# Kernel tuning notes

Hardware: AMD Instinct MI355X
Metric: run time of the kernel (lower is better)

Reference implementation:

```python
import math
import jax, jax.numpy as jnp
import numpy as np

D_MODEL = 1024
N_HEADS = 16
D_K = D_MODEL // N_HEADS
THETA = 10000.0


def setup_inputs() -> dict:
    key = jax.random.key(0)
    k1, k2, k3 = jax.random.split(key, 3)
    B, S = 2, 2048
    x = jax.random.normal(k1, (B, S, D_MODEL), dtype=jnp.float32)
    std_qkv = math.sqrt(2.0 / (D_MODEL + 3 * D_MODEL))
    std_out = math.sqrt(2.0 / (D_MODEL + D_MODEL))
    # Linear weights stored as (out_features, in_features) to match the
    # einsum '... i, o i -> ... o' contraction (trunc-normal approximated
    # by clipped normal for the reference baseline).
    w_qkv = jnp.clip(jax.random.normal(k2, (3 * D_MODEL, D_MODEL), dtype=jnp.float32) * std_qkv,
                     -3 * std_qkv, 3 * std_qkv)
    b_qkv = jnp.zeros((3 * D_MODEL,), dtype=jnp.float32)
    w_out = jnp.clip(jax.random.normal(k3, (D_MODEL, D_MODEL), dtype=jnp.float32) * std_out,
                     -3 * std_out, 3 * std_out)
    b_out = jnp.zeros((D_MODEL,), dtype=jnp.float32)
    return {"x": x, "w_qkv": w_qkv, "b_qkv": b_qkv, "w_out": w_out, "b_out": b_out}


def _rope(t, cos, sin):
    # t: (B, H, S, D_K); cos/sin: (S, D_K//2) broadcast over batch/heads.
    B, H, S, d = t.shape
    tp = t.reshape(B, H, S, d // 2, 2)
    even, odd = tp[..., 0], tp[..., 1]
    r_even = even * cos - odd * sin
    r_odd = even * sin + odd * cos
    return jnp.stack([r_even, r_odd], axis=-1).reshape(B, H, S, d)


def reference(x, w_qkv, b_qkv, w_out, b_out):
    B, S, _ = x.shape
    # QKV projection: weight is (out, in)
    qkv = jnp.einsum('bsi,oi->bso', x, w_qkv) + b_qkv  # (B, S, 3*D_MODEL)
    qkv = qkv.reshape(B, S, 3, N_HEADS, D_K).transpose(2, 0, 3, 1, 4)  # (3, B, H, S, D_K)
    q, k, v = qkv[0], qkv[1], qkv[2]

    # RoPE with default token_positions = arange(S)
    inv_freq = THETA ** (-(jnp.arange(0, D_K, 2, dtype=jnp.float32)) / D_K)  # (D_K//2,)
    ang = jnp.arange(S, dtype=jnp.float32)[:, None] * inv_freq[None, :]      # (S, D_K//2)
    cos, sin = jnp.cos(ang), jnp.sin(ang)
    q = _rope(q, cos, sin)
    k = _rope(k, cos, sin)

    # Scaled dot-product attention in fp32 with causal mask
    scale = 1.0 / math.sqrt(D_K)
    scores = jnp.einsum('bhqd,bhkd->bhqk', q.astype(jnp.float32), k.astype(jnp.float32)) * scale
    causal = jnp.tril(jnp.ones((S, S), dtype=bool))
    scores = jnp.where(causal, scores, jnp.finfo(jnp.float32).min)
    # Custom softmax: exp(x - max) / (sum + 1e-8)
    ex = jnp.exp(scores - jnp.max(scores, axis=-1, keepdims=True))
    attn = ex / (jnp.sum(ex, axis=-1, keepdims=True) + 1e-8)
    attn = attn.astype(v.dtype)

    o = jnp.einsum('bhqk,bhkd->bhqd', attn, v)           # (B, H, S, D_K)
    o = o.transpose(0, 2, 1, 3).reshape(B, S, D_MODEL)    # (B, S, D_MODEL)
    out = jnp.einsum('bsi,oi->bso', o, w_out) + b_out
    return out
```

## Files before the change

kernel.cpp:

```cpp
#include <hip/hip_runtime.h>


typedef float f32x4 __attribute__((ext_vector_type(4)));
typedef float fvec4 __attribute__((ext_vector_type(4)));
typedef __bf16 bf16x8 __attribute__((ext_vector_type(8)));
typedef unsigned int u32x4 __attribute__((ext_vector_type(4)));

#define S_SZ 2048
#define NH 16
#define DK 64

static __device__ __forceinline__ unsigned short f2bf(float f) {
  unsigned int u = __builtin_bit_cast(unsigned int, f);
  u += 0x7fffu + ((u >> 16) & 1u);
  return (unsigned short)(u >> 16);
}
static __device__ __forceinline__ float bf2f(unsigned short h) {
  unsigned int u = ((unsigned int)h) << 16;
  return __builtin_bit_cast(float, u);
}
static __device__ __forceinline__ unsigned int pk2(float a, float b) {
  return (unsigned int)f2bf(a) | ((unsigned int)f2bf(b) << 16);
}
static __device__ __forceinline__ bf16x8 ld16g(const unsigned short* p) {
  return __builtin_bit_cast(bf16x8, *(const u32x4*)p);
}
static __device__ __forceinline__ void gload_lds16(const unsigned short* g,
                                                   unsigned short* l) {
  __builtin_amdgcn_global_load_lds(
      (const __attribute__((address_space(1))) void*)g,
      (__attribute__((address_space(3))) void*)l, 16, 0, 0);
}

__global__ __launch_bounds__(256) void cvt_bf16(
    const float* __restrict__ x, const float* __restrict__ wq,
    const float* __restrict__ wo, unsigned short* __restrict__ xb,
    unsigned short* __restrict__ wqb, unsigned short* __restrict__ wob) {
  const int u = blockIdx.x * 256 + threadIdx.x;
  const float* src;
  unsigned short* dst;
  int idx;
  if (u < 524288) { src = x; dst = xb; idx = u; }
  else if (u < 917504) { src = wq; dst = wqb; idx = u - 524288; }
  else { src = wo; dst = wob; idx = u - 917504; }
  const fvec4* p = (const fvec4*)(src + (size_t)idx * 8);
  const fvec4 f0 = p[0], f1 = p[1];
  u32x4 o;
  o[0] = pk2(f0[0], f0[1]); o[1] = pk2(f0[2], f0[3]);
  o[2] = pk2(f1[0], f1[1]); o[3] = pk2(f1[2], f1[3]);
  *(u32x4*)(dst + (size_t)idx * 8) = o;
}

template <bool OBF16>
__global__ __launch_bounds__(256) void gemm_bf16(
    const unsigned short* __restrict__ A, const unsigned short* __restrict__ B,
    const float* __restrict__ bias, void* __restrict__ Cp, int N, int K) {
  __shared__ unsigned short As[2][4096];
  __shared__ unsigned short Bs[2][4096];
  const int t = threadIdx.x;
  const int lane = t & 63, w = t >> 6;
  const int lo = lane & 15, g = lane >> 4;
  const int wr = (w >> 1) * 64, wc = (w & 1) * 64;
  const int bRow = blockIdx.y * 128, bCol = blockIdx.x * 128;
  const unsigned short* ap = A + (size_t)(bRow + (t >> 2)) * K + (t & 3) * 8;
  const unsigned short* bp = B + (size_t)(bCol + (t >> 2)) * K + (t & 3) * 8;
  const size_t rK = (size_t)64 * K;
  const int wb = w * 512;
  f32x4 acc[4][4] = {};
  gload_lds16(ap, As[0] + wb);
  gload_lds16(ap + rK, As[0] + 2048 + wb);
  gload_lds16(bp, Bs[0] + wb);
  gload_lds16(bp + rK, Bs[0] + 2048 + wb);
  const int nk = K >> 5;
  for (int kt = 0; kt < nk; ++kt) {
    __syncthreads();
    if (kt + 1 < nk) {
      const int k0 = (kt + 1) << 5;
      const int nb = (kt + 1) & 1;
      gload_lds16(ap + k0, As[nb] + wb);
      gload_lds16(ap + rK + k0, As[nb] + 2048 + wb);
      gload_lds16(bp + k0, Bs[nb] + wb);
      gload_lds16(bp + rK + k0, Bs[nb] + 2048 + wb);
    }
    const unsigned short* Ac = As[kt & 1];
    const unsigned short* Bc = Bs[kt & 1];
    bf16x8 aF[4], bF[4];
#pragma unroll
    for (int m = 0; m < 4; ++m) aF[m] = ld16g(Ac + (wr + m * 16 + lo) * 32 + 8 * g);
#pragma unroll
    for (int n = 0; n < 4; ++n) bF[n] = ld16g(Bc + (wc + n * 16 + lo) * 32 + 8 * g);
    __builtin_amdgcn_s_setprio(1);
#pragma unroll
    for (int m = 0; m < 4; ++m)
#pragma unroll
      for (int n = 0; n < 4; ++n)
        acc[m][n] = __builtin_amdgcn_mfma_f32_16x16x32_bf16(aF[m], bF[n], acc[m][n], 0, 0, 0);
    __builtin_amdgcn_s_setprio(0);
  }
#pragma unroll
  for (int m = 0; m < 4; ++m) {
#pragma unroll
    for (int n = 0; n < 4; ++n) {
      const int col = bCol + wc + n * 16 + lo;
      const float bv = bias[col];
#pragma unroll
      for (int r = 0; r < 4; ++r) {
        const int row = bRow + wr + m * 16 + g * 4 + r;
        const float v = acc[m][n][r] + bv;
        if constexpr (OBF16)
          ((unsigned short*)Cp)[(size_t)row * N + col] = f2bf(v);
        else
          ((float*)Cp)[(size_t)row * N + col] = v;
      }
    }
  }
}

__global__ __launch_bounds__(256) void rope_scatter(
    const unsigned short* __restrict__ qkv, unsigned short* __restrict__ Qo,
    unsigned short* __restrict__ Ko, unsigned short* __restrict__ Vt) {
  const int t = blockIdx.x * 256 + threadIdx.x;
  const int i = t & 31;
  const int s = (t >> 5) & (S_SZ - 1);
  const int h = (t >> 16) & (NH - 1);
  const int b = t >> 20;
  const unsigned short* row = qkv + (size_t)(b * S_SZ + s) * 3072;
  const float inv = exp2f((float)i * (-13.287712379549449f / 32.0f));
  const float ang = (float)s * inv;
  float sn, cs;
  sincosf(ang, &sn, &cs);
  const unsigned int qp = *(const unsigned int*)(row + h * 64 + 2 * i);
  const unsigned int kp = *(const unsigned int*)(row + 1024 + h * 64 + 2 * i);
  const unsigned int vp = *(const unsigned int*)(row + 2048 + h * 64 + 2 * i);
  const float qe = bf2f((unsigned short)qp), qo = bf2f((unsigned short)(qp >> 16));
  const float ke = bf2f((unsigned short)kp), ko = bf2f((unsigned short)(kp >> 16));
  const size_t hb = (size_t)(b * NH + h);
  const size_t qkbase = (hb * S_SZ + s) * DK + 2 * i;
  *(unsigned int*)(Qo + qkbase) =
      pk2((qe * cs - qo * sn) * 0.125f, (qe * sn + qo * cs) * 0.125f);
  *(unsigned int*)(Ko + qkbase) = pk2(ke * cs - ko * sn, ke * sn + ko * cs);
  const size_t vb = (hb * DK + 2 * i) * S_SZ + s;
  Vt[vb] = (unsigned short)vp;
  Vt[vb + S_SZ] = (unsigned short)(vp >> 16);
}

static __device__ __forceinline__ void stage8(const unsigned short* __restrict__ gbase,
                                              int gstride, unsigned short* tile, int t) {
  const int r = t >> 3;
  const int s16 = (t & 7) ^ (r & 7);
  gload_lds16(gbase + (size_t)r * gstride + (s16 << 3), tile + (t >> 6) * 512);
}

static __device__ __forceinline__ void attn_step(
    const unsigned short* __restrict__ Kl, const unsigned short* __restrict__ Vl,
    unsigned short* __restrict__ Pw, const bf16x8 aQ0, const bf16x8 aQ1,
    const bool diag, const int wq, const int lo, const int g,
    float* __restrict__ m, float* __restrict__ lsum, f32x4* __restrict__ oacc) {
  f32x4 s[4];
  __builtin_amdgcn_s_setprio(1);
#pragma unroll
  for (int c = 0; c < 4; ++c) {
    const int kr = c * 16 + lo;
    const int sw = kr & 7;
    const bf16x8 b0 =
        __builtin_bit_cast(bf16x8, *(const u32x4*)&Kl[kr * 64 + ((g ^ sw) << 3)]);
    const bf16x8 b1 =
        __builtin_bit_cast(bf16x8, *(const u32x4*)&Kl[kr * 64 + (((4 + g) ^ sw) << 3)]);
    f32x4 z = {};
    z = __builtin_amdgcn_mfma_f32_16x16x32_bf16(aQ0, b0, z, 0, 0, 0);
    z = __builtin_amdgcn_mfma_f32_16x16x32_bf16(aQ1, b1, z, 0, 0, 0);
    s[c] = z;
  }
  __builtin_amdgcn_s_setprio(0);
  if (diag) {
#pragma unroll
    for (int c = 0; c < 4; ++c)
#pragma unroll
      for (int r = 0; r < 4; ++r)
        if ((c * 16 + lo) > (wq * 16 + g * 4 + r)) s[c][r] = -__builtin_inff();
  }
#pragma unroll
  for (int r = 0; r < 4; ++r) {
    float rm = fmaxf(fmaxf(s[0][r], s[1][r]), fmaxf(s[2][r], s[3][r]));
    rm = fmaxf(rm, __shfl_xor(rm, 1, 16));
    rm = fmaxf(rm, __shfl_xor(rm, 2, 16));
    rm = fmaxf(rm, __shfl_xor(rm, 4, 16));
    rm = fmaxf(rm, __shfl_xor(rm, 8, 16));
    const float mn = fmaxf(m[r], rm);
    const float alpha = __expf(m[r] - mn);
    m[r] = mn;
    float rs = 0.f;
#pragma unroll
    for (int c = 0; c < 4; ++c) {
      const float p = __expf(s[c][r] - mn);
      s[c][r] = p;
      rs += p;
    }
    rs += __shfl_xor(rs, 1, 16);
    rs += __shfl_xor(rs, 2, 16);
    rs += __shfl_xor(rs, 4, 16);
    rs += __shfl_xor(rs, 8, 16);
    lsum[r] = lsum[r] * alpha + rs;
#pragma unroll
    for (int nt = 0; nt < 4; ++nt) oacc[nt][r] *= alpha;
#pragma unroll
    for (int c = 0; c < 4; ++c) Pw[(g * 4 + r) * 72 + c * 16 + lo] = f2bf(s[c][r]);
  }
  __builtin_amdgcn_s_setprio(1);
#pragma unroll
  for (int kc = 0; kc < 2; ++kc) {
    const bf16x8 aP =
        __builtin_bit_cast(bf16x8, *(const u32x4*)&Pw[lo * 72 + kc * 32 + 8 * g]);
#pragma unroll
    for (int nt = 0; nt < 4; ++nt) {
      const int d = nt * 16 + lo;
      const bf16x8 bV = __builtin_bit_cast(
          bf16x8, *(const u32x4*)&Vl[d * 64 + (((kc * 4 + g) ^ (d & 7)) << 3)]);
      oacc[nt] = __builtin_amdgcn_mfma_f32_16x16x32_bf16(aP, bV, oacc[nt], 0, 0, 0);
    }
  }
  __builtin_amdgcn_s_setprio(0);
}

__global__ __launch_bounds__(512) void flash_attn(
    const unsigned short* __restrict__ Q, const unsigned short* __restrict__ K,
    const unsigned short* __restrict__ VT, unsigned short* __restrict__ O) {
  __shared__ unsigned short Kb[2][4096];
  __shared__ unsigned short Vb[2][4096];
  __shared__ unsigned short Pl[8][16 * 72];
  const int t = threadIdx.x;
  const int lane = t & 63, w = t >> 6;
  const int lo = lane & 15, g = lane >> 4;
  const int bh = blockIdx.y;
  const int j = blockIdx.x;
  const int qa = j, qb = 31 - j;
  const unsigned short* Qh = Q + (size_t)bh * S_SZ * DK;
  const unsigned short* Kh = K + (size_t)bh * S_SZ * DK;
  const unsigned short* Vh = VT + (size_t)bh * DK * S_SZ;

  const int wq = w & 3;
  const int myq = (w & 4) ? qb : qa;
  const int row = myq * 64 + wq * 16;
  const bf16x8 aQ0 = ld16g(Qh + (size_t)(row + lo) * DK + 8 * g);
  const bf16x8 aQ1 = ld16g(Qh + (size_t)(row + lo) * DK + 32 + 8 * g);

  float m[4], l[4];
  f32x4 o[4] = {};
#pragma unroll
  for (int r = 0; r < 4; ++r) { m[r] = -__builtin_inff(); l[r] = 0.f; }
  unsigned short* Pw = &Pl[w][0];

  stage8(Kh, DK, Kb[0], t);
  stage8(Vh, S_SZ, Vb[0], t);
  __syncthreads();
  int cur = 0;
  for (int kt = 0; kt <= qb; ++kt) {
    if (kt < qb) {
      const int nb = (kt + 1) * 64;
      stage8(Kh + (size_t)nb * DK, DK, Kb[cur ^ 1], t);
      stage8(Vh + nb, S_SZ, Vb[cur ^ 1], t);
    }
    if (kt <= myq)
      attn_step(Kb[cur], Vb[cur], Pw, aQ0, aQ1, kt == myq, wq, lo, g, m, l, o);
    __syncthreads();
    cur ^= 1;
  }

  const int b = bh >> 4, h = bh & 15;
#pragma unroll
  for (int r = 0; r < 4; ++r) {
    const float inv = 1.0f / (l[r] + 1e-8f);
    const size_t base = ((size_t)(b * S_SZ + row + g * 4 + r)) * 1024 + h * DK;
#pragma unroll
    for (int nt = 0; nt < 4; ++nt) O[base + nt * 16 + lo] = f2bf(o[nt][r] * inv);
  }
}

extern "C" void kernel_launch(void* const* d_in, const int* in_sizes, int n_in,
                              void* d_out, int out_size, void* d_ws, size_t ws_size,
                              hipStream_t stream) {
  const float* x = (const float*)d_in[0];
  const float* w_qkv = (const float*)d_in[1];
  const float* b_qkv = (const float*)d_in[2];
  const float* w_out = (const float*)d_in[3];
  const float* b_out = (const float*)d_in[4];
  float* out = (float*)d_out;

  char* ws = (char*)d_ws;
  unsigned short* xb = (unsigned short*)(ws);
  unsigned short* wqb = (unsigned short*)(ws + 8388608);
  unsigned short* wob = (unsigned short*)(ws + 14680064);
  unsigned short* qkv = (unsigned short*)(ws + 16777216);
  unsigned short* kb = (unsigned short*)(ws + 41943040);
  unsigned short* vt = (unsigned short*)(ws + 50331648);
  unsigned short* qb = xb;
  unsigned short* ob = qkv;

  cvt_bf16<<<4096, 256, 0, stream>>>(x, w_qkv, w_out, xb, wqb, wob);
  {
    dim3 grid(3072 / 128, 4096 / 128);
    gemm_bf16<true><<<grid, 256, 0, stream>>>(xb, wqb, b_qkv, qkv, 3072, 1024);
  }
  rope_scatter<<<(2 * NH * S_SZ * 32) / 256, 256, 0, stream>>>(qkv, qb, kb, vt);
  {
    dim3 grid(16, 2 * NH);
    flash_attn<<<grid, 512, 0, stream>>>(qb, kb, vt, ob);
  }
  {
    dim3 grid(1024 / 128, 4096 / 128);
    gemm_bf16<false><<<grid, 256, 0, stream>>>(ob, wob, b_out, out, 1024, 1024);
  }
}
```

Before: 152.9 us.

## Balance causal flash-attention work across waves, use DPP reductions and GEMM tile swizzle

The flash attention kernel now splits the long query tile's KV range between both wave groups. One group processes the first 16 KV tiles for the long tile, while the other handles the short tile and then the remaining long-tile KV tiles. Partial softmax state (m, l, o) is merged through shared memory at the end, which balances the work per wave over exactly 17 iterations and adds a second K/V staging stream plus a merge step. Row max/sum reductions switch from shfl_xor to DPP moves. The GEMM remaps block indices so consecutive workgroups are spread across XCDs, and launch bounds add a min-blocks hint.

```diff
diff --git a/kernel.cpp b/kernel.cpp
--- a/kernel.cpp
+++ b/kernel.cpp
@@ -30,6 +30,27 @@
   __builtin_amdgcn_global_load_lds(
       (const __attribute__((address_space(1))) void*)g,
       (__attribute__((address_space(3))) void*)l, 16, 0, 0);
+}
+
+template <int CTRL>
+static __device__ __forceinline__ float dppmov(float x) {
+  return __builtin_bit_cast(
+      float, __builtin_amdgcn_update_dpp(0, __builtin_bit_cast(int, x), CTRL,
+                                         0xF, 0xF, true));
+}
+static __device__ __forceinline__ float rmax16(float x) {
+  x = fmaxf(x, dppmov<0xB1>(x));
+  x = fmaxf(x, dppmov<0x4E>(x));
+  x = fmaxf(x, dppmov<0x141>(x));
+  x = fmaxf(x, dppmov<0x140>(x));
+  return x;
+}
+static __device__ __forceinline__ float rsum16(float x) {
+  x += dppmov<0xB1>(x);
+  x += dppmov<0x4E>(x);
+  x += dppmov<0x141>(x);
+  x += dppmov<0x140>(x);
+  return x;
 }
 
 __global__ __launch_bounds__(256) void cvt_bf16(
@@ -61,7 +82,12 @@
   const int lane = t & 63, w = t >> 6;
   const int lo = lane & 15, g = lane >> 4;
   const int wr = (w >> 1) * 64, wc = (w & 1) * 64;
-  const int bRow = blockIdx.y * 128, bCol = blockIdx.x * 128;
+  const int gx = gridDim.x;
+  int o = blockIdx.y * gx + blockIdx.x;
+  const int nwg = gx * gridDim.y;
+  o = (o & 7) * (nwg >> 3) + (o >> 3);
+  const int by = o / gx, bx = o - by * gx;
+  const int bRow = by * 128, bCol = bx * 128;
   const unsigned short* ap = A + (size_t)(bRow + (t >> 2)) * K + (t & 3) * 8;
   const unsigned short* bp = B + (size_t)(bCol + (t >> 2)) * K + (t & 3) * 8;
   const size_t rK = (size_t)64 * K;
@@ -182,10 +208,7 @@
 #pragma unroll
   for (int r = 0; r < 4; ++r) {
     float rm = fmaxf(fmaxf(s[0][r], s[1][r]), fmaxf(s[2][r], s[3][r]));
-    rm = fmaxf(rm, __shfl_xor(rm, 1, 16));
-    rm = fmaxf(rm, __shfl_xor(rm, 2, 16));
-    rm = fmaxf(rm, __shfl_xor(rm, 4, 16));
-    rm = fmaxf(rm, __shfl_xor(rm, 8, 16));
+    rm = rmax16(rm);
     const float mn = fmaxf(m[r], rm);
     const float alpha = __expf(m[r] - mn);
     m[r] = mn;
@@ -196,10 +219,7 @@
       s[c][r] = p;
       rs += p;
     }
-    rs += __shfl_xor(rs, 1, 16);
-    rs += __shfl_xor(rs, 2, 16);
-    rs += __shfl_xor(rs, 4, 16);
-    rs += __shfl_xor(rs, 8, 16);
+    rs = rsum16(rs);
     lsum[r] = lsum[r] * alpha + rs;
 #pragma unroll
     for (int nt = 0; nt < 4; ++nt) oacc[nt][r] *= alpha;
@@ -222,12 +242,12 @@
   __builtin_amdgcn_s_setprio(0);
 }
 
-__global__ __launch_bounds__(512) void flash_attn(
+__global__ __launch_bounds__(512, 4) void flash_attn(
     const unsigned short* __restrict__ Q, const unsigned short* __restrict__ K,
     const unsigned short* __restrict__ VT, unsigned short* __restrict__ O) {
   __shared__ unsigned short Kb[2][4096];
   __shared__ unsigned short Vb[2][4096];
-  __shared__ unsigned short Pl[8][16 * 72];
+  __shared__ unsigned short Pl[8][1152];
   const int t = threadIdx.x;
   const int lane = t & 63, w = t >> 6;
   const int lo = lane & 15, g = lane >> 4;
@@ -239,40 +259,87 @@
   const unsigned short* Vh = VT + (size_t)bh * DK * S_SZ;
 
   const int wq = w & 3;
-  const int myq = (w & 4) ? qb : qa;
-  const int row = myq * 64 + wq * 16;
-  const bf16x8 aQ0 = ld16g(Qh + (size_t)(row + lo) * DK + 8 * g);
-  const bf16x8 aQ1 = ld16g(Qh + (size_t)(row + lo) * DK + 32 + 8 * g);
-
-  float m[4], l[4];
-  f32x4 o[4] = {};
-#pragma unroll
-  for (int r = 0; r < 4; ++r) { m[r] = -__builtin_inff(); l[r] = 0.f; }
+  const bool s1 = w >= 4;
+  const int rowMain = (s1 ? qb : qa) * 64 + wq * 16;
+  const int rowB = qb * 64 + wq * 16;
+  const bf16x8 aQ0 = ld16g(Qh + (size_t)(rowMain + lo) * DK + 8 * g);
+  const bf16x8 aQ1 = ld16g(Qh + (size_t)(rowMain + lo) * DK + 32 + 8 * g);
+  bf16x8 aQB0 = aQ0, aQB1 = aQ1;
+  if (!s1) {
+    aQB0 = ld16g(Qh + (size_t)(rowB + lo) * DK + 8 * g);
+    aQB1 = ld16g(Qh + (size_t)(rowB + lo) * DK + 32 + 8 * g);
+  }
+
+  float mA[4], lA[4], mB[4], lB[4];
+  f32x4 oA[4] = {}, oB[4] = {};
+#pragma unroll
+  for (int r = 0; r < 4; ++r) {
+    mA[r] = mB[r] = -__builtin_inff();
+    lA[r] = lB[r] = 0.f;
+  }
   unsigned short* Pw = &Pl[w][0];
 
-  stage8(Kh, DK, Kb[0], t);
-  stage8(Vh, S_SZ, Vb[0], t);
-  __syncthreads();
-  int cur = 0;
-  for (int kt = 0; kt <= qb; ++kt) {
-    if (kt < qb) {
-      const int nb = (kt + 1) * 64;
-      stage8(Kh + (size_t)nb * DK, DK, Kb[cur ^ 1], t);
-      stage8(Vh + nb, S_SZ, Vb[cur ^ 1], t);
-    }
-    if (kt <= myq)
-      attn_step(Kb[cur], Vb[cur], Pw, aQ0, aQ1, kt == myq, wq, lo, g, m, l, o);
+  for (int i = 0; i <= 16; ++i) {
+    if (i < 16) {
+      stage8(Kh + (size_t)i * 64 * DK, DK, Kb[1], t);
+      stage8(Vh + i * 64, S_SZ, Vb[1], t);
+    }
+    if (i > qa) {
+      const int t0c = 15 + i - qa;
+      stage8(Kh + (size_t)t0c * 64 * DK, DK, Kb[0], t);
+      stage8(Vh + t0c * 64, S_SZ, Vb[0], t);
+    }
     __syncthreads();
-    cur ^= 1;
-  }
-
-  const int b = bh >> 4, h = bh & 15;
-#pragma unroll
-  for (int r = 0; r < 4; ++r) {
-    const float inv = 1.0f / (l[r] + 1e-8f);
-    const size_t base = ((size_t)(b * S_SZ + row + g * 4 + r)) * 1024 + h * DK;
-#pragma unroll
-    for (int nt = 0; nt < 4; ++nt) O[base + nt * 16 + lo] = f2bf(o[nt][r] * inv);
+    if (s1) {
+      if (i < 16) {
+        attn_step(Kb[1], Vb[1], Pw, aQ0, aQ1, false, wq, lo, g, mA, lA, oA);
+      } else {
+        float* ml = (float*)Pw;
+#pragma unroll
+        for (int r = 0; r < 4; ++r) {
+          ml[r * 64 + lane] = mA[r];
+          ml[(4 + r) * 64 + lane] = lA[r];
+        }
+        float* obase = (w < 6) ? ((float*)&Kb[1][0]) + (w - 4) * 1024
+                               : ((float*)&Vb[1][0]) + (w - 6) * 1024;
+#pragma unroll
+        for (int nt = 0; nt < 4; ++nt)
+#pragma unroll
+          for (int r = 0; r < 4; ++r) obase[(nt * 4 + r) * 64 + lane] = oA[nt][r];
+      }
+    } else {
+      if (i <= qa)
+        attn_step(Kb[1], Vb[1], Pw, aQ0, aQ1, i == qa, wq, lo, g, mA, lA, oA);
+      else
+        attn_step(Kb[0], Vb[0], Pw, aQB0, aQB1, i == 16, wq, lo, g, mB, lB, oB);
+    }
+    __syncthreads();
+  }
+
+  if (!s1) {
+    const int b = bh >> 4, h = bh & 15;
+#pragma unroll
+    for (int r = 0; r < 4; ++r) {
+      const float inv = 1.0f / (lA[r] + 1e-8f);
+      const size_t base = ((size_t)(b * S_SZ + rowMain + g * 4 + r)) * 1024 + h * DK;
+#pragma unroll
+      for (int nt = 0; nt < 4; ++nt) O[base + nt * 16 + lo] = f2bf(oA[nt][r] * inv);
+    }
+    const float* ml = (const float*)&Pl[w + 4][0];
+    const float* obase = (w < 2) ? ((const float*)&Kb[1][0]) + w * 1024
+                                 : ((const float*)&Vb[1][0]) + (w - 2) * 1024;
+#pragma unroll
+    for (int r = 0; r < 4; ++r) {
+      const float m1 = ml[r * 64 + lane], l1 = ml[(4 + r) * 64 + lane];
+      const float mh = fmaxf(mB[r], m1);
+      const float a0 = __expf(mB[r] - mh), a1 = __expf(m1 - mh);
+      const float linv = 1.0f / (lB[r] * a0 + l1 * a1 + 1e-8f);
+      const size_t base = ((size_t)(b * S_SZ + rowB + g * 4 + r)) * 1024 + h * DK;
+#pragma unroll
+      for (int nt = 0; nt < 4; ++nt)
+        O[base + nt * 16 + lo] =
+            f2bf((oB[nt][r] * a0 + obase[(nt * 4 + r) * 64 + lane] * a1) * linv);
+    }
   }
 }
 
```

Result: faster. 135.5 us (-11.4%).
